# Performance work log

Hardware: AMD Instinct MI355X
Metric: run time of the kernel (lower is better)

## Reference

```python
import jax, jax.numpy as jnp
import numpy as np

B, S, EH2, DH, A = 128, 1024, 1024, 512, 512

def setup_inputs() -> dict:
    key = jax.random.key(0)
    k1, k2, k3, k4, k5 = jax.random.split(key, 5)
    scale_in = 1.0 / np.sqrt(EH2 + DH)
    scale_a = 1.0 / np.sqrt(A)
    return {
        "encoder_outputs": jax.random.normal(k1, (B, S, EH2), dtype=jnp.float32),
        "decoder_hidden": jax.random.normal(k2, (B, DH), dtype=jnp.float32),
        "src_mask": jnp.ones((B, S), dtype=jnp.int32),
        "W_attn": jax.random.normal(k3, (EH2 + DH, A), dtype=jnp.float32) * scale_in,
        "b_attn": jax.random.normal(k4, (A,), dtype=jnp.float32) * scale_in,
        "v": jax.random.normal(k5, (A,), dtype=jnp.float32) * scale_a,
    }

def reference(encoder_outputs, decoder_hidden, src_mask, W_attn, b_attn, v):
    # Split W_attn into encoder-part and decoder-part to avoid materializing
    # the [B,S,EH2+DH] concat (same math as Linear(cat(enc, dec_repeated))).
    W_enc = W_attn[:EH2]          # [EH2, A]
    W_dec = W_attn[EH2:]          # [DH, A]
    enc_proj = jnp.einsum('bse,ea->bsa', encoder_outputs, W_enc)  # [B,S,A]
    dec_proj = decoder_hidden @ W_dec                              # [B,A]
    energy = jnp.tanh(enc_proj + dec_proj[:, None, :] + b_attn)    # [B,S,A]
    scores = jnp.einsum('bsa,a->bs', energy, v)                    # [B,S]
    scores = jnp.where(src_mask == 0, jnp.float32(-1e10), scores)
    attn_weights = jax.nn.softmax(scores, axis=1)                  # [B,S]
    context = jnp.einsum('bs,bse->be', attn_weights, encoder_outputs)  # [B,EH2]
    return (context, attn_weights)
```

## Files before the change

### kernel.cpp

```cpp
#include <hip/hip_runtime.h>
#include <math.h>

#define BB   128
#define SS   1024
#define EH2  1024
#define DHD  512
#define AD   512
#define MTOT (BB*SS)
#define KDIM 1024

#define BM   64
#define BK   32
#define APAD 40

typedef __attribute__((ext_vector_type(8))) short  short8;
typedef __attribute__((ext_vector_type(4))) float  f32x4;

static __device__ __forceinline__ unsigned short f2bf_rne(float x) {
    unsigned u = __float_as_uint(x);
    u += 0x7FFF + ((u >> 16) & 1);
    return (unsigned short)(u >> 16);
}

__global__ __launch_bounds__(256) void k0_wprep(
    const float* __restrict__ W, unsigned short* __restrict__ Wt)
{
    int idx = blockIdx.x * 256 + threadIdx.x;
    for (int i = idx; i < KDIM * AD; i += 512 * 256) {
        int k = i >> 9;
        int n = i & 511;
        Wt[(k >> 5) * (AD * BK) + n * BK + (k & 31)] = f2bf_rne(W[i]);
    }
}

__global__ __launch_bounds__(256) void k1_decproj(
    const float* __restrict__ dec,
    const float* __restrict__ Wdec,
    const float* __restrict__ bias,
    float* __restrict__ dec_proj)
{
    __shared__ float dls[DHD];
    const int b = blockIdx.x;
    const int t = threadIdx.x;
    for (int i = t; i < DHD; i += 256) dls[i] = dec[b * DHD + i];
    __syncthreads();
    float acc0 = bias[t];
    float acc1 = bias[t + 256];
    #pragma unroll 8
    for (int k = 0; k < DHD; ++k) {
        const float d = dls[k];
        acc0 += d * Wdec[(size_t)k * AD + t];
        acc1 += d * Wdec[(size_t)k * AD + t + 256];
    }
    dec_proj[b * AD + t]       = acc0;
    dec_proj[b * AD + t + 256] = acc1;
}

__global__ __launch_bounds__(256) void k2_gemm_score(
    const float* __restrict__ enc,
    const unsigned short* __restrict__ Wt,
    const float* __restrict__ dp,
    const float* __restrict__ v,
    float* __restrict__ scores)
{
    __shared__ unsigned short AsH[BM][APAD];
    __shared__ unsigned short AsL[BM][APAD];
    __shared__ unsigned short Bs[AD][APAD];
    __shared__ float sred[4][BM];

    const int t     = threadIdx.x;
    const int mbase = blockIdx.x * BM;
    const int b     = blockIdx.x >> 4;
    const int wave  = t >> 6;
    const int lane  = t & 63;
    const int ln    = lane & 15;
    const int kgrp  = lane >> 4;
    const int wcol  = wave * 128;

    const int arow = t >> 2;
    const int akc  = (t & 3) * 8;

    f32x4 acc[4][8];
    #pragma unroll
    for (int m = 0; m < 4; ++m)
        #pragma unroll
        for (int n = 0; n < 8; ++n) acc[m][n] = (f32x4)0.f;

    const float* encRow = enc + (size_t)(mbase + arow) * KDIM + akc;

    for (int k0 = 0; k0 < KDIM; k0 += BK) {
        __syncthreads();

        const float4 xa = *(const float4*)(encRow + k0);
        const float4 xb = *(const float4*)(encRow + k0 + 4);
        const float xs[8] = {xa.x, xa.y, xa.z, xa.w, xb.x, xb.y, xb.z, xb.w};
        short8 hi, lo;
        #pragma unroll
        for (int j = 0; j < 8; ++j) {
            const unsigned u  = __float_as_uint(xs[j]);
            hi[j] = (short)(u >> 16);
            lo[j] = (short)f2bf_rne(xs[j] - __uint_as_float(u & 0xFFFF0000u));
        }
        *(short8*)&AsH[arow][akc] = hi;
        *(short8*)&AsL[arow][akc] = lo;

        const unsigned short* wsrc = Wt + (size_t)(k0 >> 5) * (AD * BK);
        #pragma unroll
        for (int r = 0; r < 8; ++r) {
            const int flat = r * 256 + t;
            const int n  = flat >> 2;
            const int ch = (flat & 3) * 8;
            *(short8*)&Bs[n][ch] = *(const short8*)(wsrc + flat * 8);
        }
        __syncthreads();

        short8 afH[4], afL[4];
        #pragma unroll
        for (int m = 0; m < 4; ++m) {
            afH[m] = *(const short8*)&AsH[m * 16 + ln][kgrp * 8];
            afL[m] = *(const short8*)&AsL[m * 16 + ln][kgrp * 8];
        }
        #pragma unroll
        for (int n = 0; n < 8; ++n) {
            const short8 bf = *(const short8*)&Bs[wcol + n * 16 + ln][kgrp * 8];
            #pragma unroll
            for (int m = 0; m < 4; ++m) {
                acc[m][n] = __builtin_amdgcn_mfma_f32_16x16x32_bf16(afH[m], bf, acc[m][n], 0, 0, 0);
                acc[m][n] = __builtin_amdgcn_mfma_f32_16x16x32_bf16(afL[m], bf, acc[m][n], 0, 0, 0);
            }
        }
    }

    float dpv[8], vv[8];
    #pragma unroll
    for (int n = 0; n < 8; ++n) {
        const int col = wcol + n * 16 + ln;
        dpv[n] = dp[b * AD + col];
        vv[n]  = v[col];
    }
    #pragma unroll
    for (int m = 0; m < 4; ++m) {
        float s[4];
        #pragma unroll
        for (int i = 0; i < 4; ++i) {
            float sum = 0.f;
            #pragma unroll
            for (int n = 0; n < 8; ++n) {
                const float e  = acc[m][n][i] + dpv[n];
                const float t2 = __expf(2.f * e);
                sum += vv[n] * __fdividef(t2 - 1.f, t2 + 1.f);
            }
            s[i] = sum;
        }
        #pragma unroll
        for (int off = 1; off < 16; off <<= 1) {
            #pragma unroll
            for (int i = 0; i < 4; ++i) s[i] += __shfl_xor(s[i], off);
        }
        if (ln == 0) {
            f32x4 sv = {s[0], s[1], s[2], s[3]};
            *(f32x4*)&sred[wave][m * 16 + kgrp * 4] = sv;
        }
    }
    __syncthreads();
    if (t < BM)
        scores[mbase + t] = sred[0][t] + sred[1][t] + sred[2][t] + sred[3][t];
}

__global__ __launch_bounds__(256) void k3_softmax(
    const float* __restrict__ sc,
    const int*   __restrict__ mask,
    float* __restrict__ wts)
{
    const int b = blockIdx.x;
    const int t = threadIdx.x;
    float local[4];
    float mx = -3.0e38f;
    #pragma unroll
    for (int r = 0; r < 4; ++r) {
        const int s = r * 256 + t;
        float val = sc[b * SS + s];
        if (mask[b * SS + s] == 0) val = -1.0e10f;
        local[r] = val;
        mx = fmaxf(mx, val);
    }
    #pragma unroll
    for (int off = 1; off < 64; off <<= 1) mx = fmaxf(mx, __shfl_xor(mx, off));
    __shared__ float redm[4], reds[4];
    if ((t & 63) == 0) redm[t >> 6] = mx;
    __syncthreads();
    mx = fmaxf(fmaxf(redm[0], redm[1]), fmaxf(redm[2], redm[3]));

    float sum = 0.f;
    #pragma unroll
    for (int r = 0; r < 4; ++r) { local[r] = __expf(local[r] - mx); sum += local[r]; }
    #pragma unroll
    for (int off = 1; off < 64; off <<= 1) sum += __shfl_xor(sum, off);
    if ((t & 63) == 0) reds[t >> 6] = sum;
    __syncthreads();
    sum = reds[0] + reds[1] + reds[2] + reds[3];
    const float inv = 1.f / sum;
    #pragma unroll
    for (int r = 0; r < 4; ++r) wts[b * SS + r * 256 + t] = local[r] * inv;
}

#define SCHUNK 128
__global__ __launch_bounds__(256) void k4_context(
    const float* __restrict__ enc,
    const float* __restrict__ wts,
    float* __restrict__ ctx)
{
    const int b  = blockIdx.x;
    const int ch = blockIdx.y;
    const int e4 = threadIdx.x * 4;
    const float* encb = enc + (size_t)b * SS * EH2 + (size_t)ch * SCHUNK * EH2;
    const float* wb   = wts + b * SS + ch * SCHUNK;
    float4 acc = make_float4(0.f, 0.f, 0.f, 0.f);
    #pragma unroll 4
    for (int s = 0; s < SCHUNK; ++s) {
        const float w = wb[s];
        const float4 ev = *(const float4*)&encb[(size_t)s * EH2 + e4];
        acc.x = fmaf(w, ev.x, acc.x);
        acc.y = fmaf(w, ev.y, acc.y);
        acc.z = fmaf(w, ev.z, acc.z);
        acc.w = fmaf(w, ev.w, acc.w);
    }
    atomicAdd(&ctx[b * EH2 + e4 + 0], acc.x);
    atomicAdd(&ctx[b * EH2 + e4 + 1], acc.y);
    atomicAdd(&ctx[b * EH2 + e4 + 2], acc.z);
    atomicAdd(&ctx[b * EH2 + e4 + 3], acc.w);
}

extern "C" void kernel_launch(void* const* d_in, const int* in_sizes, int n_in,
                              void* d_out, int out_size, void* d_ws, size_t ws_size,
                              hipStream_t stream) {
    const float* enc    = (const float*)d_in[0];
    const float* dec    = (const float*)d_in[1];
    const int*   mask   = (const int*)  d_in[2];
    const float* W      = (const float*)d_in[3];
    const float* b_attn = (const float*)d_in[4];
    const float* v      = (const float*)d_in[5];

    float* out = (float*)d_out;
    float* ctx = out;
    float* wts = out + BB * EH2;

    unsigned short* Wt  = (unsigned short*)d_ws;
    float* dec_proj     = (float*)((char*)d_ws + (1 << 20));
    float* scores       = dec_proj + BB * AD;

    hipMemsetAsync(ctx, 0, (size_t)BB * EH2 * sizeof(float), stream);

    k0_wprep<<<512, 256, 0, stream>>>(W, Wt);

    k1_decproj<<<BB, 256, 0, stream>>>(dec, W + (size_t)EH2 * AD, b_attn, dec_proj);

    k2_gemm_score<<<MTOT / BM, 256, 0, stream>>>(enc, Wt, dec_proj, v, scores);

    k3_softmax<<<BB, 256, 0, stream>>>(scores, mask, wts);

    dim3 g4(BB, SS / SCHUNK);
    k4_context<<<g4, 256, 0, stream>>>(enc, wts, ctx);
}
```

Baseline: 1.194 ms.

## Restructure score GEMM with 32x32 MFMA, double-buffered LDS and direct global-to-LDS loads

The score GEMM now uses 128-row tiles with 512 threads. It switches to 32x32x16 bf16 MFMAs and double-buffers both A and B in LDS, so the next K-step is prefetched while the current one computes. W is pre-swizzled into the MFMA operand layout so it can be streamed with global_load_lds straight into LDS, and dp and v are staged in shared memory. This removes one barrier per K-step and exposes load latency less, at the cost of more LDS per block and a more intricate fragment layout.

```diff
diff --git a/kernel.cpp b/kernel.cpp
--- a/kernel.cpp
+++ b/kernel.cpp
@@ -9,12 +9,13 @@
 #define MTOT (BB*SS)
 #define KDIM 1024
 
-#define BM   64
-#define BK   32
-#define APAD 40
-
-typedef __attribute__((ext_vector_type(8))) short  short8;
-typedef __attribute__((ext_vector_type(4))) float  f32x4;
+#define BM2   128
+#define BK2   32
+#define NSTEP (KDIM/BK2)
+
+typedef __attribute__((ext_vector_type(8)))  short short8;
+typedef __attribute__((ext_vector_type(4)))  float f32x4;
+typedef __attribute__((ext_vector_type(16))) float f32x16;
 
 static __device__ __forceinline__ unsigned short f2bf_rne(float x) {
     unsigned u = __float_as_uint(x);
@@ -22,15 +23,24 @@
     return (unsigned short)(u >> 16);
 }
 
+#define LDS_AS(p) ((__attribute__((address_space(3))) unsigned int*)(p))
+#define GLB_AS(p) ((const __attribute__((address_space(1))) unsigned int*)(p))
+
 __global__ __launch_bounds__(256) void k0_wprep(
     const float* __restrict__ W, unsigned short* __restrict__ Wt)
 {
-    int idx = blockIdx.x * 256 + threadIdx.x;
-    for (int i = idx; i < KDIM * AD; i += 512 * 256) {
-        int k = i >> 9;
-        int n = i & 511;
-        Wt[(k >> 5) * (AD * BK) + n * BK + (k & 31)] = f2bf_rne(W[i]);
-    }
+    const int g     = blockIdx.x * 256 + threadIdx.x;
+    const int lane  = g & 63;
+    const int ct    = (g >> 6) & 15;
+    const int kk2   = (g >> 10) & 1;
+    const int ks    = g >> 11;
+    const int col   = ct * 32 + (lane & 31);
+    const int kbase = ks * 32 + kk2 * 16 + (lane >> 5) * 8;
+    short8 out;
+    #pragma unroll
+    for (int j = 0; j < 8; ++j)
+        out[j] = (short)f2bf_rne(W[(size_t)(kbase + j) * AD + col]);
+    *(short8*)&Wt[(size_t)g * 8] = out;
 }
 
 __global__ __launch_bounds__(256) void k1_decproj(
@@ -56,115 +66,153 @@
     dec_proj[b * AD + t + 256] = acc1;
 }
 
-__global__ __launch_bounds__(256) void k2_gemm_score(
+__global__ __launch_bounds__(512, 2) void k2_gemm_score(
     const float* __restrict__ enc,
     const unsigned short* __restrict__ Wt,
     const float* __restrict__ dp,
     const float* __restrict__ v,
     float* __restrict__ scores)
 {
-    __shared__ unsigned short AsH[BM][APAD];
-    __shared__ unsigned short AsL[BM][APAD];
-    __shared__ unsigned short Bs[AD][APAD];
-    __shared__ float sred[4][BM];
+    __shared__ unsigned short As[2][16][512];
+    __shared__ unsigned short Bs[2][32][512];
+    __shared__ float dp_l[AD], v_l[AD];
+    __shared__ float sred[4][BM2];
 
     const int t     = threadIdx.x;
-    const int mbase = blockIdx.x * BM;
-    const int b     = blockIdx.x >> 4;
     const int wave  = t >> 6;
     const int lane  = t & 63;
-    const int ln    = lane & 15;
-    const int kgrp  = lane >> 4;
-    const int wcol  = wave * 128;
-
-    const int arow = t >> 2;
-    const int akc  = (t & 3) * 8;
-
-    f32x4 acc[4][8];
-    #pragma unroll
-    for (int m = 0; m < 4; ++m)
+    const int mbase = blockIdx.x * BM2;
+    const int b     = blockIdx.x >> 3;
+    const int wm    = wave >> 2;
+    const int wn    = wave & 3;
+
+    dp_l[t] = dp[b * AD + t];
+    v_l[t]  = v[t];
+
+    const int smt   = (t >> 6) & 3;
+    const int skk2  = t >> 8;
+    const int srow  = smt * 32 + (lane & 31);
+    const int sksub = skk2 * 16 + (lane >> 5) * 8;
+    const float* aptr = enc + (size_t)(mbase + srow) * KDIM + sksub;
+    unsigned short* asH = &As[0][skk2 * 4 + smt][lane * 8];
+    unsigned short* asL = &As[0][(2 + skk2) * 4 + smt][lane * 8];
+    const int asStride = 16 * 512;
+
+    const unsigned short* bsrc = Wt + (size_t)wave * 2048 + (size_t)lane * 8;
+    unsigned short* bdst = &Bs[0][wave * 4][0];
+    const int bsStride = 32 * 512;
+
+#define STAGE_B(ks_, buf_) do {                                             \
+    const unsigned short* gs_ = bsrc + (size_t)(ks_) * 16384;               \
+    unsigned short* ds_ = bdst + (buf_) * bsStride;                         \
+    __builtin_amdgcn_global_load_lds(GLB_AS(gs_),        LDS_AS(ds_),        16, 0, 0); \
+    __builtin_amdgcn_global_load_lds(GLB_AS(gs_ + 512),  LDS_AS(ds_ + 512),  16, 0, 0); \
+    __builtin_amdgcn_global_load_lds(GLB_AS(gs_ + 1024), LDS_AS(ds_ + 1024), 16, 0, 0); \
+    __builtin_amdgcn_global_load_lds(GLB_AS(gs_ + 1536), LDS_AS(ds_ + 1536), 16, 0, 0); \
+} while (0)
+
+#define CONV_WRITE_A(buf_, xa_, xb_) do {                                   \
+    const float xs_[8] = {xa_.x, xa_.y, xa_.z, xa_.w, xb_.x, xb_.y, xb_.z, xb_.w}; \
+    short8 hi_, lo_;                                                        \
+    _Pragma("unroll")                                                       \
+    for (int j_ = 0; j_ < 8; ++j_) {                                        \
+        const unsigned u_ = __float_as_uint(xs_[j_]);                       \
+        hi_[j_] = (short)(u_ >> 16);                                        \
+        lo_[j_] = (short)f2bf_rne(xs_[j_] - __uint_as_float(u_ & 0xFFFF0000u)); \
+    }                                                                       \
+    *(short8*)(asH + (buf_) * asStride) = hi_;                              \
+    *(short8*)(asL + (buf_) * asStride) = lo_;                              \
+} while (0)
+
+    f32x16 acc[2][4];
+    #pragma unroll
+    for (int mi = 0; mi < 2; ++mi)
         #pragma unroll
-        for (int n = 0; n < 8; ++n) acc[m][n] = (f32x4)0.f;
-
-    const float* encRow = enc + (size_t)(mbase + arow) * KDIM + akc;
-
-    for (int k0 = 0; k0 < KDIM; k0 += BK) {
+        for (int n = 0; n < 4; ++n) acc[mi][n] = (f32x16)0.f;
+
+    STAGE_B(0, 0);
+    {
+        const float4 xa = *(const float4*)(aptr);
+        const float4 xb = *(const float4*)(aptr + 4);
+        CONV_WRITE_A(0, xa, xb);
+    }
+    __syncthreads();
+
+    int cur = 0;
+    for (int ks = 0; ks < NSTEP; ++ks) {
+        const int nxt = cur ^ 1;
+        float4 xa, xb;
+        const bool pf = (ks + 1 < NSTEP);
+        if (pf) {
+            STAGE_B(ks + 1, nxt);
+            xa = *(const float4*)(aptr + (ks + 1) * BK2);
+            xb = *(const float4*)(aptr + (ks + 1) * BK2 + 4);
+        }
+
+        #pragma unroll
+        for (int kk2 = 0; kk2 < 2; ++kk2) {
+            short8 bf[4];
+            #pragma unroll
+            for (int n = 0; n < 4; ++n)
+                bf[n] = *(const short8*)&Bs[cur][kk2 * 16 + wn * 4 + n][lane * 8];
+            #pragma unroll
+            for (int mi = 0; mi < 2; ++mi) {
+                const int mt = wm * 2 + mi;
+                const short8 aH = *(const short8*)&As[cur][kk2 * 4 + mt][lane * 8];
+                const short8 aL = *(const short8*)&As[cur][(2 + kk2) * 4 + mt][lane * 8];
+                #pragma unroll
+                for (int n = 0; n < 4; ++n) {
+                    acc[mi][n] = __builtin_amdgcn_mfma_f32_32x32x16_bf16(aH, bf[n], acc[mi][n], 0, 0, 0);
+                    acc[mi][n] = __builtin_amdgcn_mfma_f32_32x32x16_bf16(aL, bf[n], acc[mi][n], 0, 0, 0);
+                }
+            }
+        }
+
+        if (pf) CONV_WRITE_A(nxt, xa, xb);
         __syncthreads();
-
-        const float4 xa = *(const float4*)(encRow + k0);
-        const float4 xb = *(const float4*)(encRow + k0 + 4);
-        const float xs[8] = {xa.x, xa.y, xa.z, xa.w, xb.x, xb.y, xb.z, xb.w};
-        short8 hi, lo;
+        cur = nxt;
+    }
+
+    const int c    = lane & 31;
+    const int half = lane >> 5;
+    float vv[4], dpv[4];
+    #pragma unroll
+    for (int n = 0; n < 4; ++n) {
+        const int col = wn * 128 + n * 32 + c;
+        vv[n]  = v_l[col];
+        dpv[n] = dp_l[col];
+    }
+    #pragma unroll
+    for (int mi = 0; mi < 2; ++mi) {
+        const int mt = wm * 2 + mi;
+        float part[16];
         #pragma unroll
-        for (int j = 0; j < 8; ++j) {
-            const unsigned u  = __float_as_uint(xs[j]);
-            hi[j] = (short)(u >> 16);
-            lo[j] = (short)f2bf_rne(xs[j] - __uint_as_float(u & 0xFFFF0000u));
-        }
-        *(short8*)&AsH[arow][akc] = hi;
-        *(short8*)&AsL[arow][akc] = lo;
-
-        const unsigned short* wsrc = Wt + (size_t)(k0 >> 5) * (AD * BK);
-        #pragma unroll
-        for (int r = 0; r < 8; ++r) {
-            const int flat = r * 256 + t;
-            const int n  = flat >> 2;
-            const int ch = (flat & 3) * 8;
-            *(short8*)&Bs[n][ch] = *(const short8*)(wsrc + flat * 8);
-        }
-        __syncthreads();
-
-        short8 afH[4], afL[4];
-        #pragma unroll
-        for (int m = 0; m < 4; ++m) {
-            afH[m] = *(const short8*)&AsH[m * 16 + ln][kgrp * 8];
-            afL[m] = *(const short8*)&AsL[m * 16 + ln][kgrp * 8];
+        for (int r = 0; r < 16; ++r) {
+            float s = 0.f;
+            #pragma unroll
+            for (int n = 0; n < 4; ++n) {
+                const float e  = acc[mi][n][r] + dpv[n];
+                const float te = __expf(2.f * e);
+                s += vv[n] * (1.f - __fdividef(2.f, te + 1.f));
+            }
+            part[r] = s;
         }
         #pragma unroll
-        for (int n = 0; n < 8; ++n) {
-            const short8 bf = *(const short8*)&Bs[wcol + n * 16 + ln][kgrp * 8];
-            #pragma unroll
-            for (int m = 0; m < 4; ++m) {
-                acc[m][n] = __builtin_amdgcn_mfma_f32_16x16x32_bf16(afH[m], bf, acc[m][n], 0, 0, 0);
-                acc[m][n] = __builtin_amdgcn_mfma_f32_16x16x32_bf16(afL[m], bf, acc[m][n], 0, 0, 0);
-            }
+        for (int off = 1; off < 32; off <<= 1)
+            #pragma unroll
+            for (int r = 0; r < 16; ++r)
+                part[r] += __shfl_xor(part[r], off);
+        if (c == 0) {
+            #pragma unroll
+            for (int r = 0; r < 16; ++r)
+                sred[wn][mt * 32 + 4 * half + (r & 3) + 8 * (r >> 2)] = part[r];
         }
     }
-
-    float dpv[8], vv[8];
-    #pragma unroll
-    for (int n = 0; n < 8; ++n) {
-        const int col = wcol + n * 16 + ln;
-        dpv[n] = dp[b * AD + col];
-        vv[n]  = v[col];
-    }
-    #pragma unroll
-    for (int m = 0; m < 4; ++m) {
-        float s[4];
-        #pragma unroll
-        for (int i = 0; i < 4; ++i) {
-            float sum = 0.f;
-            #pragma unroll
-            for (int n = 0; n < 8; ++n) {
-                const float e  = acc[m][n][i] + dpv[n];
-                const float t2 = __expf(2.f * e);
-                sum += vv[n] * __fdividef(t2 - 1.f, t2 + 1.f);
-            }
-            s[i] = sum;
-        }
-        #pragma unroll
-        for (int off = 1; off < 16; off <<= 1) {
-            #pragma unroll
-            for (int i = 0; i < 4; ++i) s[i] += __shfl_xor(s[i], off);
-        }
-        if (ln == 0) {
-            f32x4 sv = {s[0], s[1], s[2], s[3]};
-            *(f32x4*)&sred[wave][m * 16 + kgrp * 4] = sv;
-        }
-    }
-    __syncthreads();
-    if (t < BM)
+    __syncthreads();
+    if (t < BM2)
         scores[mbase + t] = sred[0][t] + sred[1][t] + sred[2][t] + sred[3][t];
+#undef STAGE_B
+#undef CONV_WRITE_A
 }
 
 __global__ __launch_bounds__(256) void k3_softmax(
@@ -251,11 +299,11 @@
 
     hipMemsetAsync(ctx, 0, (size_t)BB * EH2 * sizeof(float), stream);
 
-    k0_wprep<<<512, 256, 0, stream>>>(W, Wt);
+    k0_wprep<<<256, 256, 0, stream>>>(W, Wt);
 
     k1_decproj<<<BB, 256, 0, stream>>>(dec, W + (size_t)EH2 * AD, b_attn, dec_proj);
 
-    k2_gemm_score<<<MTOT / BM, 256, 0, stream>>>(enc, Wt, dec_proj, v, scores);
+    k2_gemm_score<<<MTOT / BM2, 512, 0, stream>>>(enc, Wt, dec_proj, v, scores);
 
     k3_softmax<<<BB, 256, 0, stream>>>(scores, mask, wts);
 
```

After: 1.036 ms. 13.2% less time.
